# Performance work log

Hardware: AMD Instinct MI355X
Metric: run time of the kernel (lower is better)

The kernel has to match this reference:

```python
import jax, jax.numpy as jnp
import numpy as np

B, L, H, VOCAB, MAXLEN = 128, 256, 512, 32000, 256
DEPTH = 8  # L == 2**DEPTH complete binary trees

# Level offsets for internal nodes stored level-major (level 1 = just above leaves)
_OFF = np.zeros(DEPTH + 1, dtype=np.int64)
_s = 0
for _k in range(1, DEPTH + 1):
    _OFF[_k] = _s
    _s += L >> _k

# Post-order permutation of internal nodes (matches the iterative left-first
# traversal order in which the torch code appends hs)
def _post(k, j, acc):
    if k == 0:
        return
    _post(k - 1, 2 * j, acc)
    _post(k - 1, 2 * j + 1, acc)
    acc.append(int(_OFF[k]) + j)

_acc = []
_post(DEPTH, 0, _acc)
POST = np.asarray(_acc, dtype=np.int64)  # (L-1,)


def setup_inputs() -> dict:
    key = jax.random.key(0)
    ks = jax.random.split(key, 18)
    s = 1.0 / np.sqrt(H)
    d = {
        'word_idx': jax.random.randint(ks[0], (B, L), 0, VOCAB),
        'emb': jax.random.normal(ks[1], (VOCAB, H), jnp.float32) * s,
    }
    names = ['U_i_l', 'U_i_r', 'U_fl_l', 'U_fl_r', 'U_fr_l', 'U_fr_r',
             'U_o_l', 'U_o_r', 'U_c_l', 'U_c_r']
    for i, n in enumerate(names):
        d[n] = jax.random.normal(ks[2 + i], (H, H), jnp.float32) * s
    for i, n in enumerate(['b_i', 'b_fl', 'b_fr', 'b_o', 'b_c']):
        d[n] = jax.random.normal(ks[12 + i], (H,), jnp.float32) * 0.1
    return d


def reference(word_idx, emb, U_i_l, U_i_r, b_i, U_fl_l, U_fl_r, b_fl,
              U_fr_l, U_fr_r, b_fr, U_o_l, U_o_r, b_o, U_c_l, U_c_r, b_c):
    # Fuse the 5 gate projections per side into one GEMM: (5H, H)
    Wl = jnp.concatenate([U_i_l, U_fl_l, U_fr_l, U_o_l, U_c_l], axis=0)
    Wr = jnp.concatenate([U_i_r, U_fl_r, U_fr_r, U_o_r, U_c_r], axis=0)
    b = jnp.concatenate([b_i, b_fl, b_fr, b_o, b_c], axis=0)

    def combine(hl, hr, cl, cr):
        # hl/hr: (B, n, H); torch does U @ h with h (H,1) -> h @ U.T batched
        z = jnp.einsum('bnh,gh->bng', hl, Wl) + jnp.einsum('bnh,gh->bng', hr, Wr) + b
        i, fl, fr, o, c = jnp.split(z, 5, axis=-1)
        c_phr = jax.nn.sigmoid(i) * jnp.tanh(c) \
            + jax.nn.sigmoid(fl) * cl + jax.nn.sigmoid(fr) * cr
        h_phr = jax.nn.sigmoid(o) * jnp.tanh(c_phr)
        return h_phr, c_phr

    # Leaves: h = embedding row, c = 0.5 (torch: ones - 0.5)
    h = emb[word_idx]                      # (B, L, H)
    c = jnp.full((B, L, H), 0.5, emb.dtype)

    internal_hs = []
    for _ in range(DEPTH):  # level-synchronous bottom-up combine
        h, c = combine(h[:, 0::2], h[:, 1::2], c[:, 0::2], c[:, 1::2])
        internal_hs.append(h)

    H_int = jnp.concatenate(internal_hs, axis=1)  # (B, L-1, H), level-major
    post = jnp.asarray(POST)
    # torch bug faithfully reproduced: hs[0] is prepended, then all hs appended
    out = jnp.concatenate([H_int[:, post[:1]], H_int[:, post]], axis=1)  # (B, MAXLEN, H)

    forest_h = jnp.swapaxes(h, 0, 1)  # (1, B, H)
    forest_c = jnp.swapaxes(c, 0, 1)  # (1, B, H)
    return out, (forest_h, forest_c)
```

## Files before the change

### kernel.cpp

```cpp
#include <hip/hip_runtime.h>

#define NB 128
#define NL 256
#define NH 512
#define NMAX 256

typedef __attribute__((ext_vector_type(8))) short s8v;
typedef __attribute__((ext_vector_type(4))) float f4v;

struct Params {
  const int* widx;
  const float* bias[5];
  const unsigned short* wbf;
  const unsigned short* embbf;
  const unsigned short* hcprev;
  unsigned short* hcout;
  unsigned short* part;
  float* out;
  float* fh;
  float* fc;
};

struct PrepParams {
  const float* u[10];
  const float* emb;
  unsigned short* wdst;
  unsigned short* edst;
};

__device__ __forceinline__ float bf2f(unsigned short u) {
  union { unsigned int i; float f; } v;
  v.i = ((unsigned int)u) << 16;
  return v.f;
}
__device__ __forceinline__ unsigned short f2bf(float f) {
  union { float f; unsigned int i; } v;
  v.f = f;
  unsigned int x = v.i;
  x += 0x7fffu + ((x >> 16) & 1u);
  return (unsigned short)(x >> 16);
}
__device__ __forceinline__ s8v pack8(f4v a, f4v b) {
  s8v r;
  r[0] = (short)f2bf(a[0]); r[1] = (short)f2bf(a[1]);
  r[2] = (short)f2bf(a[2]); r[3] = (short)f2bf(a[3]);
  r[4] = (short)f2bf(b[0]); r[5] = (short)f2bf(b[1]);
  r[6] = (short)f2bf(b[2]); r[7] = (short)f2bf(b[3]);
  return r;
}
__device__ __forceinline__ float sigf(float x) {
  return 1.f / (1.f + __expf(-x));
}
__device__ __forceinline__ void glds16(const void* g, void* l) {
  __builtin_amdgcn_global_load_lds(
      (const __attribute__((address_space(1))) unsigned int*)g,
      (__attribute__((address_space(3))) unsigned int*)l, 16, 0, 0);
}

__global__ __launch_bounds__(256) void prep_cvt(PrepParams pp) {
  int gid = blockIdx.x * 256 + threadIdx.x;
  const float* s;
  unsigned short* d;
  if (gid < 327680) {
    int mat = gid >> 15, off = (gid & 32767) * 8;
    s = pp.u[mat] + off;
    d = pp.wdst + (size_t)mat * NH * NH + off;
  } else {
    size_t off = (size_t)(gid - 327680) * 8;
    s = pp.emb + off;
    d = pp.edst + off;
  }
  f4v x0 = *(const f4v*)s;
  f4v x1 = *(const f4v*)(s + 4);
  *(s8v*)d = pack8(x0, x1);
}


template<int LEVEL, int BM, int KS, int TILES>
__global__ __launch_bounds__(BM * 2, 2)
void lstm_level(Params p) {
  constexpr int NK = NL >> LEVEL;
  constexpr int LOGNK = 8 - LEVEL;
  constexpr int NKP = NL >> (LEVEL - 1);
  constexpr int M = NB * NK;
  constexpr int W = BM / 32;
  constexpr int ASUB = BM * 64;
  constexpr int BUFSZ = ASUB + 20480;
  constexpr int NT = 32 / KS;
  __shared__ __align__(16) unsigned char lds[2 * BUFSZ];

  const int tid = threadIdx.x;
  const int wid = tid >> 6;
  const int lane = tid & 63;
  const int lhi = lane >> 4, llo = lane & 15;
  const int mh = (BM == 256) ? (wid & 1) : 0;
  const int q  = (BM == 256) ? (wid >> 1) : wid;
  const int ht = blockIdx.y;
  const int ks = (KS > 1) ? blockIdx.z : 0;
  const int t0 = ks * NT;

  const unsigned short* abase = (LEVEL == 1) ? p.embbf : p.hcprev;

  int aOffL[2], aOffR[2];
  auto computeA = [&](int bm) {
#pragma unroll
    for (int ii = 0; ii < 2; ++ii) {
      int gi = ii * W + wid;
      int ar = gi * 16 + (lane >> 2);
      int ck = (lane & 3) ^ ((ar >> 1) & 3);
      int am = bm * BM + ar; if (am > M - 1) am = M - 1;
      int b = am >> LOGNK, j = am & (NK - 1);
      if constexpr (LEVEL == 1) {
        aOffL[ii] = p.widx[b * NL + 2 * j] * NH + ck * 8;
        aOffR[ii] = p.widx[b * NL + 2 * j + 1] * NH + ck * 8;
      } else {
        int base = (b * NKP + 2 * j) * (2 * NH);
        aOffL[ii] = base + ck * 8;
        aOffR[ii] = base + 2 * NH + ck * 8;
      }
    }
  };

  constexpr int BI = (20 + W - 1) / W;
  int bOff[BI];
#pragma unroll
  for (int ii = 0; ii < BI; ++ii) {
    int gi = ii * W + wid;
    if (gi < 20) {
      int r = gi * 16 + (lane >> 2);
      int gg = gi >> 2;
      int ck = (lane & 3) ^ ((r >> 1) & 3);
      bOff[ii] = ((2 * gg) * NH + (ht * 64 + (r & 63))) * NH + ck * 8;
    } else bOff[ii] = 0;
  }

  auto do_stage = [&](int buf, int tt) {
    unsigned char* base = lds + buf * BUFSZ;
    const int kw = (tt & 15) * 32;
    const int* ao = (tt < 16) ? aOffL : aOffR;
#pragma unroll
    for (int ii = 0; ii < 2; ++ii)
      glds16(abase + ao[ii] + kw, base + (ii * W + wid) * 1024);
    const size_t wsel = (size_t)(tt >> 4) * NH * NH;
#pragma unroll
    for (int ii = 0; ii < BI; ++ii) {
      int gi = ii * W + wid;
      if (gi < 20)
        glds16(p.wbf + wsel + bOff[ii] + kw, base + ASUB + gi * 1024);
    }
  };

  int aoff[8], boff[5];
#pragma unroll
  for (int fm = 0; fm < 8; ++fm) {
    int r = mh * 128 + fm * 16 + llo;
    aoff[fm] = r * 64 + ((lhi ^ ((r >> 1) & 3)) << 4);
  }
#pragma unroll
  for (int g = 0; g < 5; ++g) {
    int r = g * 64 + q * 16 + llo;
    boff[g] = ASUB + r * 64 + ((lhi ^ ((r >> 1) & 3)) << 4);
  }

  f4v acc[8][5];

  auto compute = [&](int buf) {
    const unsigned char* base = lds + buf * BUFSZ;
    s8v af[8], bv[5];
#pragma unroll
    for (int fm = 0; fm < 8; ++fm) af[fm] = *(const s8v*)(base + aoff[fm]);
#pragma unroll
    for (int g = 0; g < 5; ++g)  bv[g] = *(const s8v*)(base + boff[g]);
    __builtin_amdgcn_s_setprio(1);
#pragma unroll
    for (int fm = 0; fm < 8; ++fm)
#pragma unroll
      for (int g = 0; g < 5; ++g)
        acc[fm][g] = __builtin_amdgcn_mfma_f32_16x16x32_bf16(
            af[fm], bv[g], acc[fm][g], 0, 0, 0);
    __builtin_amdgcn_s_setprio(0);
  };

  const int hdl = q * 16 + llo;
  float bb[5];
#pragma unroll
  for (int g = 0; g < 5; ++g) bb[g] = p.bias[g][ht * 64 + hdl];

  int bmCur = blockIdx.x * TILES;
  computeA(bmCur);
  do_stage(0, t0);

#pragma unroll
  for (int it = 0; it < TILES; ++it) {
#pragma unroll
    for (int fm = 0; fm < 8; ++fm)
#pragma unroll
      for (int g = 0; g < 5; ++g)
        acc[fm][g] = (f4v){0.f, 0.f, 0.f, 0.f};
    __syncthreads();
    for (int t = 0; t < NT; ++t) {
      const int cur = t & 1;
      if (t + 1 < NT) do_stage(cur ^ 1, t0 + t + 1);
      compute(cur);
      if (t + 1 < NT) __syncthreads();
    }
    const int bmOut = bmCur;
    if (it + 1 < TILES) {
      bmCur = blockIdx.x * TILES + it + 1;
      computeA(bmCur);
      do_stage(0, t0);
    }

    if constexpr (KS > 1) {
#pragma unroll
      for (int fm = 0; fm < 8; ++fm) {
#pragma unroll
        for (int jj = 0; jj < 4; ++jj) {
          int m = bmOut * BM + mh * 128 + fm * 16 + lhi * 4 + jj;
          size_t base = (((size_t)(ks * M + m) * 8 + ht) * 5) * 64;
#pragma unroll
          for (int g = 0; g < 5; ++g)
            p.part[base + g * 64 + hdl] = f2bf(acc[fm][g][jj]);
        }
      }
    } else {
      const int hd = ht * 64 + hdl;
#pragma unroll
      for (int fm = 0; fm < 8; ++fm) {
#pragma unroll
        for (int jj = 0; jj < 4; ++jj) {
          int m = bmOut * BM + mh * 128 + fm * 16 + lhi * 4 + jj;
          if (m < M) {
            int b = m >> LOGNK, j = m & (NK - 1);
            float zi  = acc[fm][0][jj] + bb[0];
            float zfl = acc[fm][1][jj] + bb[1];
            float zfr = acc[fm][2][jj] + bb[2];
            float zo  = acc[fm][3][jj] + bb[3];
            float zc  = acc[fm][4][jj] + bb[4];
            float cl = 0.5f, cr = 0.5f;
            if constexpr (LEVEL > 1) {
              const unsigned short* cb =
                  p.hcprev + ((size_t)b * NKP + 2 * j) * (2 * NH) + NH;
              cl = bf2f(cb[hd]);
              cr = bf2f(cb[2 * NH + hd]);
            }
            float cnew = sigf(zi) * tanhf(zc) + sigf(zfl) * cl + sigf(zfr) * cr;
            float hnew = sigf(zo) * tanhf(cnew);
            unsigned short* orow = p.hcout + ((size_t)b * NK + j) * (2 * NH);
            orow[hd] = f2bf(hnew);
            orow[NH + hd] = f2bf(cnew);
            int colout = (((j + 1) << LEVEL) - 2 - __popc(j)) + 1;
            p.out[((size_t)b * NMAX + colout) * NH + hd] = hnew;
            if (LEVEL == 1 && j == 0) p.out[(size_t)b * NMAX * NH + hd] = hnew;
            if constexpr (LEVEL == 8) { p.fh[b * NH + hd] = hnew; p.fc[b * NH + hd] = cnew; }
          }
        }
      }
    }
  }
}

template<int LEVEL, int KS>
__global__ __launch_bounds__(256)
void lstm_combine(Params p) {
  constexpr int NK = NL >> LEVEL;
  constexpr int LOGNK = 8 - LEVEL;
  constexpr int NKP = NL >> (LEVEL - 1);
  constexpr int M = NB * NK;
  int t = blockIdx.x * 256 + threadIdx.x;
  int m = t >> 9, hd = t & 511;
  int ht = hd >> 6, hdl = hd & 63;
  int b = m >> LOGNK, j = m & (NK - 1);

  float z[5];
#pragma unroll
  for (int g = 0; g < 5; ++g) z[g] = p.bias[g][hd];
  for (int ks = 0; ks < KS; ++ks) {
    size_t base = (((size_t)(ks * M + m) * 8 + ht) * 5) * 64;
#pragma unroll
    for (int g = 0; g < 5; ++g) z[g] += bf2f(p.part[base + g * 64 + hdl]);
  }
  const unsigned short* cb = p.hcprev + ((size_t)b * NKP + 2 * j) * (2 * NH) + NH;
  float cl = bf2f(cb[hd]);
  float cr = bf2f(cb[2 * NH + hd]);
  float cnew = sigf(z[0]) * tanhf(z[4]) + sigf(z[1]) * cl + sigf(z[2]) * cr;
  float hnew = sigf(z[3]) * tanhf(cnew);
  unsigned short* orow = p.hcout + ((size_t)b * NK + j) * (2 * NH);
  orow[hd] = f2bf(hnew);
  orow[NH + hd] = f2bf(cnew);
  int colout = (((j + 1) << LEVEL) - 2 - __popc(j)) + 1;
  p.out[((size_t)b * NMAX + colout) * NH + hd] = hnew;
  if constexpr (LEVEL == 8) { p.fh[b * NH + hd] = hnew; p.fc[b * NH + hd] = cnew; }
}

extern "C" void kernel_launch(void* const* d_in, const int* in_sizes, int n_in,
                              void* d_out, int out_size, void* d_ws, size_t ws_size,
                              hipStream_t stream) {
  unsigned short* wbf = (unsigned short*)d_ws;
  unsigned short* R1  = wbf + (size_t)10 * NH * NH;
  unsigned short* R2  = R1 + 16777216;

  PrepParams pp;
  for (int i = 0; i < 10; ++i) pp.u[i] = (const float*)d_in[2 + i];
  pp.emb  = (const float*)d_in[1];
  pp.wdst = wbf;
  pp.edst = R1;

  Params p;
  p.widx = (const int*)d_in[0];
  for (int g = 0; g < 5; ++g) p.bias[g] = (const float*)d_in[12 + g];
  p.wbf   = wbf;
  p.embbf = R1;
  p.part  = nullptr;
  p.out   = (float*)d_out;
  p.fh    = p.out + (size_t)NB * NMAX * NH;
  p.fc    = p.fh + NB * NH;

  prep_cvt<<<dim3(9280), dim3(256), 0, stream>>>(pp);

  unsigned short* lvlout[9];
  for (int k = 1; k <= 8; ++k) lvlout[k] = (k & 1) ? R2 : R1;

  p.hcprev = nullptr;     p.hcout = lvlout[1];
  lstm_level<1, 128, 1, 2><<<dim3(64, 8), dim3(256), 0, stream>>>(p);
  p.hcprev = lvlout[1];   p.hcout = lvlout[2];
  lstm_level<2, 128, 1, 1><<<dim3(64, 8), dim3(256), 0, stream>>>(p);
  p.hcprev = lvlout[2];   p.hcout = lvlout[3];
  lstm_level<3, 128, 1, 1><<<dim3(32, 8), dim3(256), 0, stream>>>(p);

  p.hcprev = lvlout[3];   p.hcout = lvlout[4];
  p.part   = lvlout[3] + 6 * 1024 * 1024;
  lstm_level<4, 128, 2, 1><<<dim3(16, 8, 2), dim3(256), 0, stream>>>(p);
  lstm_combine<4, 2><<<dim3(4096), dim3(256), 0, stream>>>(p);

  p.hcprev = lvlout[4];   p.hcout = lvlout[5];
  p.part   = lvlout[4] + 4 * 1024 * 1024;
  lstm_level<5, 128, 4, 1><<<dim3(8, 8, 4), dim3(256), 0, stream>>>(p);
  lstm_combine<5, 4><<<dim3(2048), dim3(256), 0, stream>>>(p);

  p.hcprev = lvlout[5];   p.hcout = lvlout[6];
  p.part   = lvlout[5] + 4 * 1024 * 1024;
  lstm_level<6, 128, 4, 1><<<dim3(4, 8, 4), dim3(256), 0, stream>>>(p);
  lstm_combine<6, 4><<<dim3(1024), dim3(256), 0, stream>>>(p);

  p.hcprev = lvlout[6];   p.hcout = lvlout[7];
  p.part   = lvlout[6] + 4 * 1024 * 1024;
  lstm_level<7, 128, 8, 1><<<dim3(2, 8, 8), dim3(256), 0, stream>>>(p);
  lstm_combine<7, 8><<<dim3(512), dim3(256), 0, stream>>>(p);

  p.hcprev = lvlout[7];   p.hcout = lvlout[8];
  p.part   = lvlout[7] + 4 * 1024 * 1024;
  lstm_level<8, 128, 8, 1><<<dim3(1, 8, 8), dim3(256), 0, stream>>>(p);
  lstm_combine<8, 8><<<dim3(256), dim3(256), 0, stream>>>(p);
}
```

Baseline: 305.6 us.

## Load weight fragments directly into registers instead of staging through LDS

The weight (B operand) tiles are no longer copied into shared memory. Each lane now loads its own MFMA B fragment straight from global memory into registers, double-buffered across K-steps, and the loop is unrolled by two to alternate register buffers. This shrinks the LDS footprint and removes the shared-memory write/read traffic for weights, which may allow higher occupancy. The BM==256 two-M-half split (mh) is dropped, so weight loads are no longer shared across waves through LDS, and global load latency must be hidden by the register prefetch.

```diff
diff --git a/kernel.cpp b/kernel.cpp
--- a/kernel.cpp
+++ b/kernel.cpp
@@ -84,8 +84,7 @@
   constexpr int NKP = NL >> (LEVEL - 1);
   constexpr int M = NB * NK;
   constexpr int W = BM / 32;
-  constexpr int ASUB = BM * 64;
-  constexpr int BUFSZ = ASUB + 20480;
+  constexpr int BUFSZ = BM * 64;
   constexpr int NT = 32 / KS;
   __shared__ __align__(16) unsigned char lds[2 * BUFSZ];
 
@@ -93,8 +92,7 @@
   const int wid = tid >> 6;
   const int lane = tid & 63;
   const int lhi = lane >> 4, llo = lane & 15;
-  const int mh = (BM == 256) ? (wid & 1) : 0;
-  const int q  = (BM == 256) ? (wid >> 1) : wid;
+  const int q  = wid;
   const int ht = blockIdx.y;
   const int ks = (KS > 1) ? blockIdx.z : 0;
   const int t0 = ks * NT;
@@ -121,19 +119,6 @@
     }
   };
 
-  constexpr int BI = (20 + W - 1) / W;
-  int bOff[BI];
-#pragma unroll
-  for (int ii = 0; ii < BI; ++ii) {
-    int gi = ii * W + wid;
-    if (gi < 20) {
-      int r = gi * 16 + (lane >> 2);
-      int gg = gi >> 2;
-      int ck = (lane & 3) ^ ((r >> 1) & 3);
-      bOff[ii] = ((2 * gg) * NH + (ht * 64 + (r & 63))) * NH + ck * 8;
-    } else bOff[ii] = 0;
-  }
-
   auto do_stage = [&](int buf, int tt) {
     unsigned char* base = lds + buf * BUFSZ;
     const int kw = (tt & 15) * 32;
@@ -141,36 +126,33 @@
 #pragma unroll
     for (int ii = 0; ii < 2; ++ii)
       glds16(abase + ao[ii] + kw, base + (ii * W + wid) * 1024);
-    const size_t wsel = (size_t)(tt >> 4) * NH * NH;
-#pragma unroll
-    for (int ii = 0; ii < BI; ++ii) {
-      int gi = ii * W + wid;
-      if (gi < 20)
-        glds16(p.wbf + wsel + bOff[ii] + kw, base + ASUB + gi * 1024);
-    }
   };
 
-  int aoff[8], boff[5];
+  size_t bOffG[5];
+#pragma unroll
+  for (int g = 0; g < 5; ++g)
+    bOffG[g] = (size_t)(2 * g) * NH * NH
+             + (size_t)(ht * 64 + q * 16 + llo) * NH + lhi * 8;
+  auto loadB = [&](s8v* dst, int tt) {
+    const unsigned short* src = p.wbf + (size_t)(tt >> 4) * NH * NH + (tt & 15) * 32;
+#pragma unroll
+    for (int g = 0; g < 5; ++g) dst[g] = *(const s8v*)(src + bOffG[g]);
+  };
+
+  int aoff[8];
 #pragma unroll
   for (int fm = 0; fm < 8; ++fm) {
-    int r = mh * 128 + fm * 16 + llo;
+    int r = fm * 16 + llo;
     aoff[fm] = r * 64 + ((lhi ^ ((r >> 1) & 3)) << 4);
   }
-#pragma unroll
-  for (int g = 0; g < 5; ++g) {
-    int r = g * 64 + q * 16 + llo;
-    boff[g] = ASUB + r * 64 + ((lhi ^ ((r >> 1) & 3)) << 4);
-  }
 
   f4v acc[8][5];
 
-  auto compute = [&](int buf) {
+  auto computeR = [&](int buf, const s8v* bv) {
     const unsigned char* base = lds + buf * BUFSZ;
-    s8v af[8], bv[5];
+    s8v af[8];
 #pragma unroll
     for (int fm = 0; fm < 8; ++fm) af[fm] = *(const s8v*)(base + aoff[fm]);
-#pragma unroll
-    for (int g = 0; g < 5; ++g)  bv[g] = *(const s8v*)(base + boff[g]);
     __builtin_amdgcn_s_setprio(1);
 #pragma unroll
     for (int fm = 0; fm < 8; ++fm)
@@ -186,9 +168,11 @@
 #pragma unroll
   for (int g = 0; g < 5; ++g) bb[g] = p.bias[g][ht * 64 + hdl];
 
+  s8v bva[5], bvb[5];
   int bmCur = blockIdx.x * TILES;
   computeA(bmCur);
   do_stage(0, t0);
+  loadB(bva, t0);
 
 #pragma unroll
   for (int it = 0; it < TILES; ++it) {
@@ -198,17 +182,22 @@
       for (int g = 0; g < 5; ++g)
         acc[fm][g] = (f4v){0.f, 0.f, 0.f, 0.f};
     __syncthreads();
-    for (int t = 0; t < NT; ++t) {
-      const int cur = t & 1;
-      if (t + 1 < NT) do_stage(cur ^ 1, t0 + t + 1);
-      compute(cur);
-      if (t + 1 < NT) __syncthreads();
+    for (int t = 0; t < NT; t += 2) {
+      if (t + 1 < NT) { do_stage(1, t0 + t + 1); loadB(bvb, t0 + t + 1); }
+      computeR(0, bva);
+      if (t + 1 < NT) {
+        __syncthreads();
+        if (t + 2 < NT) { do_stage(0, t0 + t + 2); loadB(bva, t0 + t + 2); }
+        computeR(1, bvb);
+        if (t + 2 < NT) __syncthreads();
+      }
     }
     const int bmOut = bmCur;
     if (it + 1 < TILES) {
       bmCur = blockIdx.x * TILES + it + 1;
       computeA(bmCur);
       do_stage(0, t0);
+      loadB(bva, t0);
     }
 
     if constexpr (KS > 1) {
@@ -216,7 +205,7 @@
       for (int fm = 0; fm < 8; ++fm) {
 #pragma unroll
         for (int jj = 0; jj < 4; ++jj) {
-          int m = bmOut * BM + mh * 128 + fm * 16 + lhi * 4 + jj;
+          int m = bmOut * BM + fm * 16 + lhi * 4 + jj;
           size_t base = (((size_t)(ks * M + m) * 8 + ht) * 5) * 64;
 #pragma unroll
           for (int g = 0; g < 5; ++g)
@@ -229,7 +218,7 @@
       for (int fm = 0; fm < 8; ++fm) {
 #pragma unroll
         for (int jj = 0; jj < 4; ++jj) {
-          int m = bmOut * BM + mh * 128 + fm * 16 + lhi * 4 + jj;
+          int m = bmOut * BM + fm * 16 + lhi * 4 + jj;
           if (m < M) {
             int b = m >> LOGNK, j = m & (NK - 1);
             float zi  = acc[fm][0][jj] + bb[0];
```

New measurement: 353.9 us. 15.8% more time.

## Stage GEMM tiles through registers with two-deep prefetch for first three levels

Applied to the files above, without the earlier changes.

Adds a register-staged pipeline variant for levels 1-3. Global tiles are loaded into VGPRs two steps ahead and then written to LDS with ds_write, replacing the direct global-to-LDS glds16 loads. The MFMA compute is also split into two halves of four A fragments each, which lowers the number of live fragment registers. The aim is to hide global latency better on the large early levels, at the cost of more register pressure and an extra sync per step.

```diff
diff --git a/kernel.cpp b/kernel.cpp
--- a/kernel.cpp
+++ b/kernel.cpp
@@ -76,7 +76,7 @@
 }
 
 
-template<int LEVEL, int BM, int KS, int TILES>
+template<int LEVEL, int BM, int KS, int TILES, int RS>
 __global__ __launch_bounds__(BM * 2, 2)
 void lstm_level(Params p) {
   constexpr int NK = NL >> LEVEL;
@@ -150,6 +150,30 @@
     }
   };
 
+  s8v aR[2], bR[BI];
+  auto loadRegs = [&](int tt) {
+    const int kw = (tt & 15) * 32;
+    const int* ao = (tt < 16) ? aOffL : aOffR;
+    aR[0] = *(const s8v*)(abase + ao[0] + kw);
+    aR[1] = *(const s8v*)(abase + ao[1] + kw);
+    const size_t wsel = (size_t)(tt >> 4) * NH * NH;
+#pragma unroll
+    for (int ii = 0; ii < BI; ++ii) {
+      int gi = ii * W + wid;
+      if (gi < 20) bR[ii] = *(const s8v*)(p.wbf + wsel + bOff[ii] + kw);
+    }
+  };
+  auto dsWrite = [&](int buf) {
+    unsigned char* base = lds + buf * BUFSZ;
+    *(s8v*)(base + (0 * W + wid) * 1024 + lane * 16) = aR[0];
+    *(s8v*)(base + (1 * W + wid) * 1024 + lane * 16) = aR[1];
+#pragma unroll
+    for (int ii = 0; ii < BI; ++ii) {
+      int gi = ii * W + wid;
+      if (gi < 20) *(s8v*)(base + ASUB + gi * 1024 + lane * 16) = bR[ii];
+    }
+  };
+
   int aoff[8], boff[5];
 #pragma unroll
   for (int fm = 0; fm < 8; ++fm) {
@@ -166,19 +190,24 @@
 
   auto compute = [&](int buf) {
     const unsigned char* base = lds + buf * BUFSZ;
-    s8v af[8], bv[5];
-#pragma unroll
-    for (int fm = 0; fm < 8; ++fm) af[fm] = *(const s8v*)(base + aoff[fm]);
-#pragma unroll
-    for (int g = 0; g < 5; ++g)  bv[g] = *(const s8v*)(base + boff[g]);
-    __builtin_amdgcn_s_setprio(1);
-#pragma unroll
-    for (int fm = 0; fm < 8; ++fm)
-#pragma unroll
-      for (int g = 0; g < 5; ++g)
-        acc[fm][g] = __builtin_amdgcn_mfma_f32_16x16x32_bf16(
-            af[fm], bv[g], acc[fm][g], 0, 0, 0);
-    __builtin_amdgcn_s_setprio(0);
+    s8v bv[5];
+#pragma unroll
+    for (int g = 0; g < 5; ++g) bv[g] = *(const s8v*)(base + boff[g]);
+#pragma unroll
+    for (int half = 0; half < 2; ++half) {
+      s8v af[4];
+#pragma unroll
+      for (int f2 = 0; f2 < 4; ++f2)
+        af[f2] = *(const s8v*)(base + aoff[half * 4 + f2]);
+      __builtin_amdgcn_s_setprio(1);
+#pragma unroll
+      for (int f2 = 0; f2 < 4; ++f2)
+#pragma unroll
+        for (int g = 0; g < 5; ++g)
+          acc[half * 4 + f2][g] = __builtin_amdgcn_mfma_f32_16x16x32_bf16(
+              af[f2], bv[g], acc[half * 4 + f2][g], 0, 0, 0);
+      __builtin_amdgcn_s_setprio(0);
+    }
   };
 
   const int hdl = q * 16 + llo;
@@ -186,31 +215,7 @@
 #pragma unroll
   for (int g = 0; g < 5; ++g) bb[g] = p.bias[g][ht * 64 + hdl];
 
-  int bmCur = blockIdx.x * TILES;
-  computeA(bmCur);
-  do_stage(0, t0);
-
-#pragma unroll
-  for (int it = 0; it < TILES; ++it) {
-#pragma unroll
-    for (int fm = 0; fm < 8; ++fm)
-#pragma unroll
-      for (int g = 0; g < 5; ++g)
-        acc[fm][g] = (f4v){0.f, 0.f, 0.f, 0.f};
-    __syncthreads();
-    for (int t = 0; t < NT; ++t) {
-      const int cur = t & 1;
-      if (t + 1 < NT) do_stage(cur ^ 1, t0 + t + 1);
-      compute(cur);
-      if (t + 1 < NT) __syncthreads();
-    }
-    const int bmOut = bmCur;
-    if (it + 1 < TILES) {
-      bmCur = blockIdx.x * TILES + it + 1;
-      computeA(bmCur);
-      do_stage(0, t0);
-    }
-
+  auto epilogue = [&](int bmOut) {
     if constexpr (KS > 1) {
 #pragma unroll
       for (int fm = 0; fm < 8; ++fm) {
@@ -257,6 +262,58 @@
         }
       }
     }
+  };
+
+  if constexpr (RS) {
+#pragma unroll
+    for (int it = 0; it < TILES; ++it) {
+      const int bm = blockIdx.x * TILES + it;
+      computeA(bm);
+      loadRegs(t0);
+#pragma unroll
+      for (int fm = 0; fm < 8; ++fm)
+#pragma unroll
+        for (int g = 0; g < 5; ++g)
+          acc[fm][g] = (f4v){0.f, 0.f, 0.f, 0.f};
+      __syncthreads();
+      dsWrite(0);
+      loadRegs(t0 + 1);
+      __syncthreads();
+      for (int t = 0; t < NT; ++t) {
+        const int cur = t & 1;
+        if (t + 1 < NT) dsWrite(cur ^ 1);
+        if (t + 2 < NT) loadRegs(t0 + t + 2);
+        compute(cur);
+        __syncthreads();
+      }
+      epilogue(bm);
+    }
+  } else {
+    int bmCur = blockIdx.x * TILES;
+    computeA(bmCur);
+    do_stage(0, t0);
+#pragma unroll
+    for (int it = 0; it < TILES; ++it) {
+#pragma unroll
+      for (int fm = 0; fm < 8; ++fm)
+#pragma unroll
+        for (int g = 0; g < 5; ++g)
+          acc[fm][g] = (f4v){0.f, 0.f, 0.f, 0.f};
+      __syncthreads();
+      for (int t = 0; t < NT; ++t) {
+        const int cur = t & 1;
+        if (t + 1 < NT) do_stage(cur ^ 1, t0 + t + 1);
+        compute(cur);
+        if (t + 1 < NT) __syncthreads();
+      }
+      const int bmOut = bmCur;
+      if (it + 1 < TILES) {
+        bmCur = blockIdx.x * TILES + it + 1;
+        computeA(bmCur);
+        do_stage(0, t0);
+      }
+      epilogue(bmOut);
+    }
   }
 }
 
@@ -322,34 +379,34 @@
   for (int k = 1; k <= 8; ++k) lvlout[k] = (k & 1) ? R2 : R1;
 
   p.hcprev = nullptr;     p.hcout = lvlout[1];
-  lstm_level<1, 128, 1, 2><<<dim3(64, 8), dim3(256), 0, stream>>>(p);
+  lstm_level<1, 128, 1, 2, 1><<<dim3(64, 8), dim3(256), 0, stream>>>(p);
   p.hcprev = lvlout[1];   p.hcout = lvlout[2];
-  lstm_level<2, 128, 1, 1><<<dim3(64, 8), dim3(256), 0, stream>>>(p);
+  lstm_level<2, 128, 1, 1, 1><<<dim3(64, 8), dim3(256), 0, stream>>>(p);
   p.hcprev = lvlout[2];   p.hcout = lvlout[3];
-  lstm_level<3, 128, 1, 1><<<dim3(32, 8), dim3(256), 0, stream>>>(p);
+  lstm_level<3, 128, 1, 1, 1><<<dim3(32, 8), dim3(256), 0, stream>>>(p);
 
   p.hcprev = lvlout[3];   p.hcout = lvlout[4];
   p.part   = lvlout[3] + 6 * 1024 * 1024;
-  lstm_level<4, 128, 2, 1><<<dim3(16, 8, 2), dim3(256), 0, stream>>>(p);
+  lstm_level<4, 128, 2, 1, 0><<<dim3(16, 8, 2), dim3(256), 0, stream>>>(p);
   lstm_combine<4, 2><<<dim3(4096), dim3(256), 0, stream>>>(p);
 
   p.hcprev = lvlout[4];   p.hcout = lvlout[5];
   p.part   = lvlout[4] + 4 * 1024 * 1024;
-  lstm_level<5, 128, 4, 1><<<dim3(8, 8, 4), dim3(256), 0, stream>>>(p);
+  lstm_level<5, 128, 4, 1, 0><<<dim3(8, 8, 4), dim3(256), 0, stream>>>(p);
   lstm_combine<5, 4><<<dim3(2048), dim3(256), 0, stream>>>(p);
 
   p.hcprev = lvlout[5];   p.hcout = lvlout[6];
   p.part   = lvlout[5] + 4 * 1024 * 1024;
-  lstm_level<6, 128, 4, 1><<<dim3(4, 8, 4), dim3(256), 0, stream>>>(p);
+  lstm_level<6, 128, 4, 1, 0><<<dim3(4, 8, 4), dim3(256), 0, stream>>>(p);
   lstm_combine<6, 4><<<dim3(1024), dim3(256), 0, stream>>>(p);
 
   p.hcprev = lvlout[6];   p.hcout = lvlout[7];
   p.part   = lvlout[6] + 4 * 1024 * 1024;
-  lstm_level<7, 128, 8, 1><<<dim3(2, 8, 8), dim3(256), 0, stream>>>(p);
+  lstm_level<7, 128, 8, 1, 0><<<dim3(2, 8, 8), dim3(256), 0, stream>>>(p);
   lstm_combine<7, 8><<<dim3(512), dim3(256), 0, stream>>>(p);
 
   p.hcprev = lvlout[7];   p.hcout = lvlout[8];
   p.part   = lvlout[7] + 4 * 1024 * 1024;
-  lstm_level<8, 128, 8, 1><<<dim3(1, 8, 8), dim3(256), 0, stream>>>(p);
+  lstm_level<8, 128, 8, 1, 0><<<dim3(1, 8, 8), dim3(256), 0, stream>>>(p);
   lstm_combine<8, 8><<<dim3(256), dim3(256), 0, stream>>>(p);
 }
```

Result: slower. 324.2 us (+6.1%).
